# Kernel tuning notes

Measured on AMD Instinct MI355X. Metric: run time of the kernel, lower is better.

## Reference

```python
import jax, jax.numpy as jnp
import numpy as np

B, S, D, H, HID = 8192, 16, 128, 8, 1024
DH = D // H  # 16
GCN, NUMF = 40, 103
EPS = 1e-5

def _make_pe():
    pos = np.arange(S, dtype=np.float64)[:, None]
    i = np.arange(D, dtype=np.float64)[None, :]
    pe = pos / np.power(10000.0, (i // 2 * 2.0) / D)
    pe[:, 0::2] = np.sin(pe[:, 0::2])
    pe[:, 1::2] = np.cos(pe[:, 1::2])
    return jnp.asarray(pe, dtype=jnp.float32)  # [S, D]

PE = _make_pe()

def setup_inputs() -> dict:
    key = jax.random.key(0)
    ks = jax.random.split(key, 16)
    rn = lambda k, shape, s=0.02: (jax.random.normal(k, shape, jnp.float32) * s)
    return {
        "x": jax.random.normal(ks[0], (B, S, D), jnp.float32),
        "gcn_i": jax.random.normal(ks[1], (B, GCN), jnp.float32),
        "num": jax.random.normal(ks[2], (B, NUMF), jnp.float32),
        # two independent encoder layers, params stacked on leading dim
        "Wq": rn(ks[3], (2, D, D)), "bq": jnp.zeros((2, D), jnp.float32),
        "Wk": rn(ks[4], (2, D, D)), "bk": jnp.zeros((2, D), jnp.float32),
        "Wv": rn(ks[5], (2, D, D)), "bv": jnp.zeros((2, D), jnp.float32),
        "Wo": rn(ks[6], (2, D, D)), "bo": jnp.zeros((2, D), jnp.float32),
        "ln1_g": jnp.ones((2, D), jnp.float32), "ln1_b": jnp.zeros((2, D), jnp.float32),
        "W1": rn(ks[7], (2, D, HID)), "b1": jnp.zeros((2, HID), jnp.float32),
        "W2": rn(ks[8], (2, HID, D)), "b2": jnp.zeros((2, D), jnp.float32),
        "ln2_g": jnp.ones((2, D), jnp.float32), "ln2_b": jnp.zeros((2, D), jnp.float32),
        # head
        "Wn": rn(ks[9], (NUMF, D)), "bnum": jnp.zeros((D,), jnp.float32),
        "bn_gamma": jnp.ones((D,), jnp.float32), "bn_beta": jnp.zeros((D,), jnp.float32),
        "Wf": rn(ks[10], (S * D + GCN + D, 1)), "bf": jnp.zeros((1,), jnp.float32),
    }

def _ln(x, g, b):
    m = x.mean(-1, keepdims=True)
    v = ((x - m) ** 2).mean(-1, keepdims=True)
    return (x - m) * jax.lax.rsqrt(v + EPS) * g + b

def reference(x, gcn_i, num, Wq, bq, Wk, bk, Wv, bv, Wo, bo, ln1_g, ln1_b,
              W1, b1, W2, b2, ln2_g, ln2_b, Wn, bnum, bn_gamma, bn_beta, Wf, bf):
    out = x + PE  # positional encoding (dropout = identity in eval)
    scale = DH ** -0.5
    for l in range(2):
        # NOTE: original uses a raw .view(B*H, -1, DH) (no transpose) -- faithful reshape
        q = (out @ Wq[l] + bq[l]).reshape(B * H, S, DH)
        k = (out @ Wk[l] + bk[l]).reshape(B * H, S, DH)
        v = (out @ Wv[l] + bv[l]).reshape(B * H, S, DH)
        attn = jax.nn.softmax(jnp.einsum('nsd,ntd->nst', q, k) * scale, axis=-1)
        ctx = jnp.einsum('nst,ntd->nsd', attn, v).reshape(B, S, D)
        h = _ln(ctx @ Wo[l] + bo[l] + out, ln1_g[l], ln1_b[l])
        ff = jax.nn.relu(h @ W1[l] + b1[l]) @ W2[l] + b2[l]
        out = _ln(ff + h, ln2_g[l], ln2_b[l])
    flat = out.reshape(B, S * D)  # [B, 2048]
    n = num @ Wn + bnum  # [B, 128]
    # BatchNorm1d, training-mode forward (biased batch variance)
    mu = n.mean(0)
    var = ((n - mu) ** 2).mean(0)
    n = (n - mu) * jax.lax.rsqrt(var + EPS) * bn_gamma + bn_beta
    p = jnp.concatenate([flat, gcn_i, n], axis=-1)  # [B, 2216]
    return jax.nn.sigmoid(p @ Wf + bf)
```

## Files before the change

kernel.cpp:

```cpp
#include <hip/hip_runtime.h>
#include <hip/hip_bf16.h>
#include <math.h>

#define B_SZ   8192
#define S_SZ   16
#define D_SZ   128
#define HID_SZ 1024
#define NUMF_SZ 103
#define GCN_SZ 40
#define G_B    4
#define NBLK   (B_SZ / G_B)
#define STRD   136

typedef short bh8 __attribute__((ext_vector_type(8)));
typedef float fx4 __attribute__((ext_vector_type(4)));

__device__ __forceinline__ fx4 mfma16(bh8 a, bh8 b, fx4 c) {
    return __builtin_amdgcn_mfma_f32_16x16x32_bf16(a, b, c, 0, 0, 0);
}

__device__ __forceinline__ unsigned short f2b(float f) {
    unsigned u = __float_as_uint(f);
    return (unsigned short)((u + 0x7fffu + ((u >> 16) & 1u)) >> 16);
}
__device__ __forceinline__ float bu2f(unsigned short u) {
    return __uint_as_float(((unsigned)u) << 16);
}

__global__ __launch_bounds__(256) void prep_weights(
    const float* __restrict__ Wq, const float* __restrict__ Wk,
    const float* __restrict__ Wv, const float* __restrict__ Wo,
    const float* __restrict__ W1, const float* __restrict__ W2,
    unsigned short* __restrict__ WswQ, unsigned short* __restrict__ WswK,
    unsigned short* __restrict__ WswV, unsigned short* __restrict__ WswO,
    unsigned short* __restrict__ Wsw1, unsigned short* __restrict__ Wsw2,
    float* __restrict__ PEt)
{
    int i = blockIdx.x * 256 + threadIdx.x;
    if (i < 2048) {
        int s = i >> 7, c = i & 127;
        float expo = (float)((c >> 1) * 2) * (1.0f / 128.0f);
        float denom = powf(10000.0f, expo);
        float ang = (float)s / denom;
        PEt[i] = (c & 1) ? cosf(ang) : sinf(ang);
    }
    if (i < 2 * 16384) {
        int l = i >> 14, r = i & 16383;
        int nt = r >> 11, ks = (r >> 9) & 3, lane = (r >> 3) & 63, e = r & 7;
        int k = ks * 32 + (lane >> 4) * 8 + e;
        int n = nt * 16 + (lane & 15);
        int s = l * 16384 + k * 128 + n;
        WswQ[i] = f2b(Wq[s]); WswK[i] = f2b(Wk[s]);
        WswV[i] = f2b(Wv[s]); WswO[i] = f2b(Wo[s]);
    }
    {
        int l = i >> 17, r = i & 131071;
        int nt = r >> 11, ks = (r >> 9) & 3, lane = (r >> 3) & 63, e = r & 7;
        int k = ks * 32 + (lane >> 4) * 8 + e;
        int n = nt * 16 + (lane & 15);
        Wsw1[i] = f2b(W1[l * 131072 + k * 1024 + n]);
    }
    {
        int l = i >> 17, r = i & 131071;
        int nt = r >> 14, kt = (r >> 9) & 31, lane = (r >> 3) & 63, e = r & 7;
        int k = kt * 32 + (lane >> 4) * 8 + e;
        int n = nt * 16 + (lane & 15);
        Wsw2[i] = f2b(W2[l * 131072 + k * 128 + n]);
    }
}

__global__ __launch_bounds__(256, 2) void encoder_fused(
    const float* __restrict__ x, const float* __restrict__ gcn,
    const float* __restrict__ bq, const float* __restrict__ bk,
    const float* __restrict__ bv, const float* __restrict__ bo,
    const float* __restrict__ ln1g, const float* __restrict__ ln1b,
    const float* __restrict__ b1, const float* __restrict__ b2p,
    const float* __restrict__ ln2g, const float* __restrict__ ln2b,
    const float* __restrict__ Wf,
    const unsigned short* __restrict__ WswQ, const unsigned short* __restrict__ WswK,
    const unsigned short* __restrict__ WswV, const unsigned short* __restrict__ WswO,
    const unsigned short* __restrict__ Wsw1, const unsigned short* __restrict__ Wsw2,
    const float* __restrict__ PEt,
    float* __restrict__ acc1)
{
    __shared__ unsigned short ACT[64][STRD];
    __shared__ unsigned short Qb[64][STRD];
    __shared__ unsigned short Kb[64][STRD];
    __shared__ unsigned short Vb[64][STRD];
    __shared__ float LNp[64][4][2];
    __shared__ float LNs[64][2];

    const int t = threadIdx.x;
    const int w = t >> 6, lane = t & 63;
    const int q = lane >> 4, ln = lane & 15;
    const int bbase = blockIdx.x * G_B;

    {
        const float4* xb = (const float4*)(x + (size_t)bbase * 2048);
        const float4* pe4 = (const float4*)PEt;
#pragma unroll
        for (int i = 0; i < 8; ++i) {
            int f4 = i * 256 + t;
            float4 xv = xb[f4];
            float4 pv = pe4[f4 & 511];
            int flat = f4 * 4;
            int row = flat >> 7, col = flat & 127;
            ushort4 pk = {f2b(xv.x + pv.x), f2b(xv.y + pv.y),
                          f2b(xv.z + pv.z), f2b(xv.w + pv.w)};
            *(ushort4*)&ACT[row][col] = pk;
        }
    }
    __syncthreads();

    for (int l = 0; l < 2; ++l) {
        {
            bh8 afr[4][4];
#pragma unroll
            for (int mt = 0; mt < 4; ++mt)
#pragma unroll
                for (int ks = 0; ks < 4; ++ks)
                    afr[mt][ks] = *(const bh8*)&ACT[mt * 16 + ln][ks * 32 + q * 8];
            const unsigned short* Wm[3] = {WswQ + l * 16384, WswK + l * 16384, WswV + l * 16384};
            const float* bias3[3] = {bq + l * 128, bk + l * 128, bv + l * 128};
#pragma unroll
            for (int mtx = 0; mtx < 3; ++mtx) {
                unsigned short (*dst)[STRD] = (mtx == 0) ? Qb : (mtx == 1) ? Kb : Vb;
#pragma unroll
                for (int i2 = 0; i2 < 2; ++i2) {
                    int nt = w * 2 + i2;
                    bh8 wfr[4];
#pragma unroll
                    for (int ks = 0; ks < 4; ++ks)
                        wfr[ks] = *(const bh8*)(Wm[mtx] + ((nt * 4 + ks) * 64 + lane) * 8);
                    int n = nt * 16 + ln;
                    float bb = bias3[mtx][n];
#pragma unroll
                    for (int mt = 0; mt < 4; ++mt) {
                        fx4 acc = {0.f, 0.f, 0.f, 0.f};
#pragma unroll
                        for (int ks = 0; ks < 4; ++ks) acc = mfma16(afr[mt][ks], wfr[ks], acc);
#pragma unroll
                        for (int r2 = 0; r2 < 4; ++r2)
                            dst[mt * 16 + q * 4 + r2][n] = f2b(acc[r2] + bb);
                    }
                }
            }
        }
        __syncthreads();

        {
            int base = w * 16;
            int g = lane >> 3, u0 = (lane & 7) * 2;
            float qr[2][16];
#pragma unroll
            for (int h = 0; h < 2; ++h) {
                int u = u0 + h;
                int qsr = base + 2 * g + (u >> 3), qc = (u & 7) * 16;
                bh8 a0 = *(const bh8*)&Qb[qsr][qc];
                bh8 a1 = *(const bh8*)&Qb[qsr][qc + 8];
#pragma unroll
                for (int e = 0; e < 8; ++e) {
                    qr[h][e] = bu2f((unsigned short)a0[e]);
                    qr[h][8 + e] = bu2f((unsigned short)a1[e]);
                }
            }
            float p[2][16];
#pragma unroll
            for (int tp = 0; tp < 16; ++tp) {
                int ksr = base + 2 * g + (tp >> 3), kc = (tp & 7) * 16;
                bh8 k0 = *(const bh8*)&Kb[ksr][kc];
                bh8 k1 = *(const bh8*)&Kb[ksr][kc + 8];
                float d0 = 0.f, d1 = 0.f;
#pragma unroll
                for (int e = 0; e < 8; ++e) {
                    float kv = bu2f((unsigned short)k0[e]);
                    d0 = fmaf(qr[0][e], kv, d0); d1 = fmaf(qr[1][e], kv, d1);
                }
#pragma unroll
                for (int e = 0; e < 8; ++e) {
                    float kv = bu2f((unsigned short)k1[e]);
                    d0 = fmaf(qr[0][8 + e], kv, d0); d1 = fmaf(qr[1][8 + e], kv, d1);
                }
                p[0][tp] = d0 * 0.25f; p[1][tp] = d1 * 0.25f;
            }
#pragma unroll
            for (int h = 0; h < 2; ++h) {
                float mx = -1e30f;
#pragma unroll
                for (int tp = 0; tp < 16; ++tp) mx = fmaxf(mx, p[h][tp]);
                float sum = 0.f;
#pragma unroll
                for (int tp = 0; tp < 16; ++tp) { p[h][tp] = __expf(p[h][tp] - mx); sum += p[h][tp]; }
                float is = 1.0f / sum;
#pragma unroll
                for (int tp = 0; tp < 16; ++tp) p[h][tp] *= is;
            }
            float ctx[2][16];
#pragma unroll
            for (int h = 0; h < 2; ++h)
#pragma unroll
                for (int e = 0; e < 16; ++e) ctx[h][e] = 0.f;
#pragma unroll
            for (int tp = 0; tp < 16; ++tp) {
                int vsr = base + 2 * g + (tp >> 3), vc = (tp & 7) * 16;
                bh8 v0 = *(const bh8*)&Vb[vsr][vc];
                bh8 v1 = *(const bh8*)&Vb[vsr][vc + 8];
#pragma unroll
                for (int e = 0; e < 8; ++e) {
                    float vv = bu2f((unsigned short)v0[e]);
                    ctx[0][e] = fmaf(p[0][tp], vv, ctx[0][e]);
                    ctx[1][e] = fmaf(p[1][tp], vv, ctx[1][e]);
                }
#pragma unroll
                for (int e = 0; e < 8; ++e) {
                    float vv = bu2f((unsigned short)v1[e]);
                    ctx[0][8 + e] = fmaf(p[0][tp], vv, ctx[0][8 + e]);
                    ctx[1][8 + e] = fmaf(p[1][tp], vv, ctx[1][8 + e]);
                }
            }
#pragma unroll
            for (int h = 0; h < 2; ++h) {
                int u = u0 + h;
                int s = base + 2 * g + (u >> 3), dc = (u & 7) * 16;
                bh8 c0, c1;
#pragma unroll
                for (int e = 0; e < 8; ++e) {
                    c0[e] = (short)f2b(ctx[h][e]);
                    c1[e] = (short)f2b(ctx[h][8 + e]);
                }
                *(bh8*)&Qb[s][dc] = c0;
                *(bh8*)&Qb[s][dc + 8] = c1;
            }
        }
        __syncthreads();

        fx4 Cv[2][4];
        {
            bh8 cfr[4][4];
#pragma unroll
            for (int mt = 0; mt < 4; ++mt)
#pragma unroll
                for (int ks = 0; ks < 4; ++ks)
                    cfr[mt][ks] = *(const bh8*)&Qb[mt * 16 + ln][ks * 32 + q * 8];
#pragma unroll
            for (int i2 = 0; i2 < 2; ++i2) {
                int nt = w * 2 + i2, n = nt * 16 + ln;
                bh8 wfr[4];
#pragma unroll
                for (int ks = 0; ks < 4; ++ks)
                    wfr[ks] = *(const bh8*)(WswO + l * 16384 + ((nt * 4 + ks) * 64 + lane) * 8);
                float bb = bo[l * 128 + n];
#pragma unroll
                for (int mt = 0; mt < 4; ++mt) {
                    fx4 acc = {0.f, 0.f, 0.f, 0.f};
#pragma unroll
                    for (int ks = 0; ks < 4; ++ks) acc = mfma16(cfr[mt][ks], wfr[ks], acc);
#pragma unroll
                    for (int r2 = 0; r2 < 4; ++r2)
                        Cv[i2][mt][r2] = acc[r2] + bb +
                            bu2f(ACT[mt * 16 + q * 4 + r2][n]);
                }
            }
        }
#pragma unroll
        for (int mt = 0; mt < 4; ++mt) {
            float s4[4], v4[4];
#pragma unroll
            for (int r2 = 0; r2 < 4; ++r2) {
                float a0 = Cv[0][mt][r2], a1 = Cv[1][mt][r2];
                float s = a0 + a1, v = a0 * a0 + a1 * a1;
#pragma unroll
                for (int m = 1; m < 16; m <<= 1) { s += __shfl_xor(s, m); v += __shfl_xor(v, m); }
                s4[r2] = s; v4[r2] = v;
            }
            if (ln < 8)
                LNp[mt * 16 + q * 4 + (ln >> 1)][w][ln & 1] = (ln & 1) ? v4[ln >> 1] : s4[ln >> 1];
        }
        __syncthreads();
        if (t < 64) {
            float s = LNp[t][0][0] + LNp[t][1][0] + LNp[t][2][0] + LNp[t][3][0];
            float v = LNp[t][0][1] + LNp[t][1][1] + LNp[t][2][1] + LNp[t][3][1];
            float mean = s * (1.0f / 128.0f);
            LNs[t][0] = mean;
            LNs[t][1] = rsqrtf(v * (1.0f / 128.0f) - mean * mean + 1e-5f);
        }
        __syncthreads();
#pragma unroll
        for (int i2 = 0; i2 < 2; ++i2) {
            int n = (w * 2 + i2) * 16 + ln;
            float gg = ln1g[l * 128 + n], be = ln1b[l * 128 + n];
#pragma unroll
            for (int mt = 0; mt < 4; ++mt)
#pragma unroll
                for (int r2 = 0; r2 < 4; ++r2) {
                    int row = mt * 16 + q * 4 + r2;
                    Kb[row][n] = f2b((Cv[i2][mt][r2] - LNs[row][0]) * LNs[row][1] * gg + be);
                }
        }
        __syncthreads();

        bh8 hfr[4][4];
#pragma unroll
        for (int mt = 0; mt < 4; ++mt)
#pragma unroll
            for (int ks = 0; ks < 4; ++ks)
                hfr[mt][ks] = *(const bh8*)&Kb[mt * 16 + ln][ks * 32 + q * 8];
        fx4 f2a[2][4];
#pragma unroll
        for (int i2 = 0; i2 < 2; ++i2)
#pragma unroll
            for (int mt = 0; mt < 4; ++mt) f2a[i2][mt] = fx4{0.f, 0.f, 0.f, 0.f};
        for (int ch = 0; ch < 8; ++ch) {
            bh8 w1fr[2][4];
#pragma unroll
            for (int i2 = 0; i2 < 2; ++i2) {
                int ntg = ch * 8 + w * 2 + i2;
#pragma unroll
                for (int ks = 0; ks < 4; ++ks)
                    w1fr[i2][ks] = *(const bh8*)(Wsw1 + l * 131072 + ((ntg * 4 + ks) * 64 + lane) * 8);
            }
#pragma unroll
            for (int mt = 0; mt < 4; ++mt) {
#pragma unroll
                for (int i2 = 0; i2 < 2; ++i2) {
                    fx4 acc = {0.f, 0.f, 0.f, 0.f};
#pragma unroll
                    for (int ks = 0; ks < 4; ++ks) acc = mfma16(hfr[mt][ks], w1fr[i2][ks], acc);
                    int nl = (w * 2 + i2) * 16 + ln;
                    float bb = b1[l * HID_SZ + ch * 128 + nl];
#pragma unroll
                    for (int r2 = 0; r2 < 4; ++r2) {
                        float vv = acc[r2] + bb;
                        Qb[mt * 16 + q * 4 + r2][nl] = f2b(vv > 0.f ? vv : 0.f);
                    }
                }
            }
            __syncthreads();
            bh8 w2fr[2][4];
#pragma unroll
            for (int i2 = 0; i2 < 2; ++i2)
#pragma unroll
                for (int ks = 0; ks < 4; ++ks)
                    w2fr[i2][ks] = *(const bh8*)(Wsw2 + l * 131072 +
                        (((w * 2 + i2) * 32 + ch * 4 + ks) * 64 + lane) * 8);
#pragma unroll
            for (int mt = 0; mt < 4; ++mt) {
                bh8 ffr[4];
#pragma unroll
                for (int ks = 0; ks < 4; ++ks)
                    ffr[ks] = *(const bh8*)&Qb[mt * 16 + ln][ks * 32 + q * 8];
#pragma unroll
                for (int i2 = 0; i2 < 2; ++i2)
#pragma unroll
                    for (int ks = 0; ks < 4; ++ks)
                        f2a[i2][mt] = mfma16(ffr[ks], w2fr[i2][ks], f2a[i2][mt]);
            }
            __syncthreads();
        }
        fx4 Cv2[2][4];
#pragma unroll
        for (int i2 = 0; i2 < 2; ++i2) {
            int n = (w * 2 + i2) * 16 + ln;
            float bb = b2p[l * 128 + n];
#pragma unroll
            for (int mt = 0; mt < 4; ++mt)
#pragma unroll
                for (int r2 = 0; r2 < 4; ++r2)
                    Cv2[i2][mt][r2] = f2a[i2][mt][r2] + bb +
                        bu2f(Kb[mt * 16 + q * 4 + r2][n]);
        }
#pragma unroll
        for (int mt = 0; mt < 4; ++mt) {
            float s4[4], v4[4];
#pragma unroll
            for (int r2 = 0; r2 < 4; ++r2) {
                float a0 = Cv2[0][mt][r2], a1 = Cv2[1][mt][r2];
                float s = a0 + a1, v = a0 * a0 + a1 * a1;
#pragma unroll
                for (int m = 1; m < 16; m <<= 1) { s += __shfl_xor(s, m); v += __shfl_xor(v, m); }
                s4[r2] = s; v4[r2] = v;
            }
            if (ln < 8)
                LNp[mt * 16 + q * 4 + (ln >> 1)][w][ln & 1] = (ln & 1) ? v4[ln >> 1] : s4[ln >> 1];
        }
        __syncthreads();
        if (t < 64) {
            float s = LNp[t][0][0] + LNp[t][1][0] + LNp[t][2][0] + LNp[t][3][0];
            float v = LNp[t][0][1] + LNp[t][1][1] + LNp[t][2][1] + LNp[t][3][1];
            float mean = s * (1.0f / 128.0f);
            LNs[t][0] = mean;
            LNs[t][1] = rsqrtf(v * (1.0f / 128.0f) - mean * mean + 1e-5f);
        }
        __syncthreads();
#pragma unroll
        for (int i2 = 0; i2 < 2; ++i2) {
            int n = (w * 2 + i2) * 16 + ln;
            float gg = ln2g[l * 128 + n], be = ln2b[l * 128 + n];
#pragma unroll
            for (int mt = 0; mt < 4; ++mt)
#pragma unroll
                for (int r2 = 0; r2 < 4; ++r2) {
                    int row = mt * 16 + q * 4 + r2;
                    ACT[row][n] = f2b((Cv2[i2][mt][r2] - LNs[row][0]) * LNs[row][1] * gg + be);
                }
        }
        __syncthreads();
    }

    {
        int bg = bbase + w;
        float part = 0.f;
        int srow = lane >> 2, c0 = (lane & 3) * 32;
#pragma unroll
        for (int i = 0; i < 4; ++i) {
            bh8 av = *(const bh8*)&ACT[w * 16 + srow][c0 + i * 8];
            int fl = srow * 128 + c0 + i * 8;
#pragma unroll
            for (int e = 0; e < 8; ++e)
                part = fmaf(bu2f((unsigned short)av[e]), Wf[fl + e], part);
        }
        if (lane < GCN_SZ)
            part = fmaf(gcn[(size_t)bg * GCN_SZ + lane], Wf[2048 + lane], part);
#pragma unroll
        for (int off = 32; off; off >>= 1) part += __shfl_xor(part, off);
        if (lane == 0) acc1[bg] = part;
    }
}

__global__ __launch_bounds__(256) void num_stats_kernel(
    const float* __restrict__ num, const float* __restrict__ Wn,
    const float* __restrict__ bnum,
    float* __restrict__ ssum, float* __restrict__ ssq)
{
    __shared__ float NUM[16][NUMF_SZ + 1];
    __shared__ float cred[4][128];
    const int t = threadIdx.x;
    const int b0 = blockIdx.x * 16;
    const int j = t & 127, sg = t >> 7, s0 = sg * 8;

    for (int idx = t; idx < 16 * NUMF_SZ; idx += 256) {
        int r = idx / NUMF_SZ, f = idx - r * NUMF_SZ;
        NUM[r][f] = num[(size_t)(b0 + r) * NUMF_SZ + f];
    }
    __syncthreads();

    float acc[8];
    float bnv = bnum[j];
#pragma unroll
    for (int r = 0; r < 8; ++r) acc[r] = bnv;
    for (int f = 0; f < NUMF_SZ; ++f) {
        float w = Wn[f * 128 + j];
#pragma unroll
        for (int r = 0; r < 8; ++r) acc[r] = fmaf(NUM[s0 + r][f], w, acc[r]);
    }
    float lsum = 0.f, lsq = 0.f;
#pragma unroll
    for (int r = 0; r < 8; ++r) {
        lsum += acc[r];
        lsq = fmaf(acc[r], acc[r], lsq);
    }
    cred[sg][j] = lsum;
    cred[2 + sg][j] = lsq;
    __syncthreads();
    if (sg == 0) atomicAdd(&ssum[j], cred[0][j] + cred[1][j]);
    else         atomicAdd(&ssq[j],  cred[2][j] + cred[3][j]);
}

__global__ __launch_bounds__(128) void final_kernel(
    const float* __restrict__ num, const float* __restrict__ Wn,
    const float* __restrict__ bnum,
    const float* __restrict__ ssum, const float* __restrict__ ssq,
    const float* __restrict__ gamma, const float* __restrict__ beta,
    const float* __restrict__ Wf, const float* __restrict__ bfin,
    const float* __restrict__ acc1, float* __restrict__ out)
{
    const int b = blockIdx.x, jj = threadIdx.x;
    __shared__ float red2[2];
    __shared__ float NUMr[NUMF_SZ];
    if (jj < NUMF_SZ) NUMr[jj] = num[(size_t)b * NUMF_SZ + jj];
    __syncthreads();

    float nv = bnum[jj];
    for (int f = 0; f < NUMF_SZ; ++f)
        nv = fmaf(NUMr[f], Wn[f * 128 + jj], nv);

    float mean = ssum[jj] * (1.0f / (float)B_SZ);
    float var = ssq[jj] * (1.0f / (float)B_SZ) - mean * mean;
    float bnv = (nv - mean) * rsqrtf(var + 1e-5f) * gamma[jj] + beta[jj];
    float v = bnv * Wf[2088 + jj];
#pragma unroll
    for (int o = 32; o; o >>= 1) v += __shfl_down(v, o);
    if ((jj & 63) == 0) red2[jj >> 6] = v;
    __syncthreads();
    if (jj == 0) {
        float z = acc1[b] + red2[0] + red2[1] + bfin[0];
        out[b] = 1.0f / (1.0f + __expf(-z));
    }
}

extern "C" void kernel_launch(void* const* d_in, const int* in_sizes, int n_in,
                              void* d_out, int out_size, void* d_ws, size_t ws_size,
                              hipStream_t stream)
{
    const float* x    = (const float*)d_in[0];
    const float* gcn  = (const float*)d_in[1];
    const float* num  = (const float*)d_in[2];
    const float* Wq   = (const float*)d_in[3];
    const float* bq   = (const float*)d_in[4];
    const float* Wk   = (const float*)d_in[5];
    const float* bk   = (const float*)d_in[6];
    const float* Wv   = (const float*)d_in[7];
    const float* bv   = (const float*)d_in[8];
    const float* Wo   = (const float*)d_in[9];
    const float* bo   = (const float*)d_in[10];
    const float* ln1g = (const float*)d_in[11];
    const float* ln1b = (const float*)d_in[12];
    const float* W1   = (const float*)d_in[13];
    const float* b1   = (const float*)d_in[14];
    const float* W2   = (const float*)d_in[15];
    const float* b2p  = (const float*)d_in[16];
    const float* ln2g = (const float*)d_in[17];
    const float* ln2b = (const float*)d_in[18];
    const float* Wn   = (const float*)d_in[19];
    const float* bnum = (const float*)d_in[20];
    const float* bng  = (const float*)d_in[21];
    const float* bnb  = (const float*)d_in[22];
    const float* Wf   = (const float*)d_in[23];
    const float* bfin = (const float*)d_in[24];

    float* acc1 = (float*)d_ws;
    float* ssum = acc1 + B_SZ;
    float* ssq  = ssum + 128;
    unsigned short* wb = (unsigned short*)((char*)d_ws + 40960);
    unsigned short* WswQ = wb;
    unsigned short* WswK = wb + 32768;
    unsigned short* WswV = wb + 65536;
    unsigned short* WswO = wb + 98304;
    unsigned short* Wsw1 = wb + 131072;
    unsigned short* Wsw2 = wb + 393216;
    float* PEt = (float*)((char*)d_ws + 40960 + 1310720);

    hipMemsetAsync(ssum, 0, 2 * 128 * sizeof(float), stream);
    prep_weights<<<1024, 256, 0, stream>>>(Wq, Wk, Wv, Wo, W1, W2,
        WswQ, WswK, WswV, WswO, Wsw1, Wsw2, PEt);
    encoder_fused<<<NBLK, 256, 0, stream>>>(x, gcn, bq, bk, bv, bo,
        ln1g, ln1b, b1, b2p, ln2g, ln2b, Wf,
        WswQ, WswK, WswV, WswO, Wsw1, Wsw2, PEt, acc1);
    num_stats_kernel<<<B_SZ / 16, 256, 0, stream>>>(num, Wn, bnum, ssum, ssq);
    final_kernel<<<B_SZ, 128, 0, stream>>>(num, Wn, bnum, ssum, ssq, bng, bnb,
        Wf, bfin, acc1, (float*)d_out);
}
```

Before: 491.1 us.

## Drop ACT LDS buffer, keep residual in registers, merge stats into prep

The encoder kernel drops its separate ACT shared buffer and reuses Qb for the activations. The residual is kept in registers (rsd), and the LN statistics reuse LNp, which cuts LDS use enough to raise launch bounds from 2 to 3 blocks per CU. The numeric-feature BatchNorm statistics kernel is folded into the weight-prep launch as extra blocks, and the final kernel now handles 8 rows per block instead of 1. The aim is higher occupancy and fewer, fatter launches, at the risk of register spills under the tighter 3-block bound and an extra sync per layer.

```diff
diff --git a/kernel.cpp b/kernel.cpp
--- a/kernel.cpp
+++ b/kernel.cpp
@@ -27,49 +27,86 @@
     return __uint_as_float(((unsigned)u) << 16);
 }
 
-__global__ __launch_bounds__(256) void prep_weights(
+__global__ __launch_bounds__(256) void prep_and_stats(
     const float* __restrict__ Wq, const float* __restrict__ Wk,
     const float* __restrict__ Wv, const float* __restrict__ Wo,
     const float* __restrict__ W1, const float* __restrict__ W2,
+    const float* __restrict__ num, const float* __restrict__ Wn,
+    const float* __restrict__ bnum,
     unsigned short* __restrict__ WswQ, unsigned short* __restrict__ WswK,
     unsigned short* __restrict__ WswV, unsigned short* __restrict__ WswO,
     unsigned short* __restrict__ Wsw1, unsigned short* __restrict__ Wsw2,
-    float* __restrict__ PEt)
+    float* __restrict__ PEt, float* __restrict__ ssum, float* __restrict__ ssq)
 {
-    int i = blockIdx.x * 256 + threadIdx.x;
-    if (i < 2048) {
-        int s = i >> 7, c = i & 127;
-        float expo = (float)((c >> 1) * 2) * (1.0f / 128.0f);
-        float denom = powf(10000.0f, expo);
-        float ang = (float)s / denom;
-        PEt[i] = (c & 1) ? cosf(ang) : sinf(ang);
-    }
-    if (i < 2 * 16384) {
-        int l = i >> 14, r = i & 16383;
-        int nt = r >> 11, ks = (r >> 9) & 3, lane = (r >> 3) & 63, e = r & 7;
-        int k = ks * 32 + (lane >> 4) * 8 + e;
-        int n = nt * 16 + (lane & 15);
-        int s = l * 16384 + k * 128 + n;
-        WswQ[i] = f2b(Wq[s]); WswK[i] = f2b(Wk[s]);
-        WswV[i] = f2b(Wv[s]); WswO[i] = f2b(Wo[s]);
-    }
-    {
-        int l = i >> 17, r = i & 131071;
-        int nt = r >> 11, ks = (r >> 9) & 3, lane = (r >> 3) & 63, e = r & 7;
-        int k = ks * 32 + (lane >> 4) * 8 + e;
-        int n = nt * 16 + (lane & 15);
-        Wsw1[i] = f2b(W1[l * 131072 + k * 1024 + n]);
-    }
-    {
-        int l = i >> 17, r = i & 131071;
-        int nt = r >> 14, kt = (r >> 9) & 31, lane = (r >> 3) & 63, e = r & 7;
-        int k = kt * 32 + (lane >> 4) * 8 + e;
-        int n = nt * 16 + (lane & 15);
-        Wsw2[i] = f2b(W2[l * 131072 + k * 128 + n]);
-    }
-}
-
-__global__ __launch_bounds__(256, 2) void encoder_fused(
+    if (blockIdx.x < 1024) {
+        int i = blockIdx.x * 256 + threadIdx.x;
+        if (i < 2048) {
+            int s = i >> 7, c = i & 127;
+            float expo = (float)((c >> 1) * 2) * (1.0f / 128.0f);
+            float denom = powf(10000.0f, expo);
+            float ang = (float)s / denom;
+            PEt[i] = (c & 1) ? cosf(ang) : sinf(ang);
+        }
+        if (i < 2 * 16384) {
+            int l = i >> 14, r = i & 16383;
+            int nt = r >> 11, ks = (r >> 9) & 3, lane = (r >> 3) & 63, e = r & 7;
+            int k = ks * 32 + (lane >> 4) * 8 + e;
+            int n = nt * 16 + (lane & 15);
+            int s = l * 16384 + k * 128 + n;
+            WswQ[i] = f2b(Wq[s]); WswK[i] = f2b(Wk[s]);
+            WswV[i] = f2b(Wv[s]); WswO[i] = f2b(Wo[s]);
+        }
+        {
+            int l = i >> 17, r = i & 131071;
+            int nt = r >> 11, ks = (r >> 9) & 3, lane = (r >> 3) & 63, e = r & 7;
+            int k = ks * 32 + (lane >> 4) * 8 + e;
+            int n = nt * 16 + (lane & 15);
+            Wsw1[i] = f2b(W1[l * 131072 + k * 1024 + n]);
+        }
+        {
+            int l = i >> 17, r = i & 131071;
+            int nt = r >> 14, kt = (r >> 9) & 31, lane = (r >> 3) & 63, e = r & 7;
+            int k = kt * 32 + (lane >> 4) * 8 + e;
+            int n = nt * 16 + (lane & 15);
+            Wsw2[i] = f2b(W2[l * 131072 + k * 128 + n]);
+        }
+    } else {
+        __shared__ float NUM[16][NUMF_SZ + 1];
+        __shared__ float cred[4][128];
+        const int t = threadIdx.x;
+        const int b0 = (blockIdx.x - 1024) * 16;
+        const int j = t & 127, sg = t >> 7, s0 = sg * 8;
+
+        for (int idx = t; idx < 16 * NUMF_SZ; idx += 256) {
+            int r = idx / NUMF_SZ, f = idx - r * NUMF_SZ;
+            NUM[r][f] = num[(size_t)(b0 + r) * NUMF_SZ + f];
+        }
+        __syncthreads();
+
+        float acc[8];
+        float bnv = bnum[j];
+#pragma unroll
+        for (int r = 0; r < 8; ++r) acc[r] = bnv;
+        for (int f = 0; f < NUMF_SZ; ++f) {
+            float w = Wn[f * 128 + j];
+#pragma unroll
+            for (int r = 0; r < 8; ++r) acc[r] = fmaf(NUM[s0 + r][f], w, acc[r]);
+        }
+        float lsum = 0.f, lsq = 0.f;
+#pragma unroll
+        for (int r = 0; r < 8; ++r) {
+            lsum += acc[r];
+            lsq = fmaf(acc[r], acc[r], lsq);
+        }
+        cred[sg][j] = lsum;
+        cred[2 + sg][j] = lsq;
+        __syncthreads();
+        if (sg == 0) atomicAdd(&ssum[j], cred[0][j] + cred[1][j]);
+        else         atomicAdd(&ssq[j],  cred[2][j] + cred[3][j]);
+    }
+}
+
+__global__ __launch_bounds__(256, 3) void encoder_fused(
     const float* __restrict__ x, const float* __restrict__ gcn,
     const float* __restrict__ bq, const float* __restrict__ bk,
     const float* __restrict__ bv, const float* __restrict__ bo,
@@ -83,12 +120,10 @@
     const float* __restrict__ PEt,
     float* __restrict__ acc1)
 {
-    __shared__ unsigned short ACT[64][STRD];
     __shared__ unsigned short Qb[64][STRD];
     __shared__ unsigned short Kb[64][STRD];
     __shared__ unsigned short Vb[64][STRD];
     __shared__ float LNp[64][4][2];
-    __shared__ float LNs[64][2];
 
     const int t = threadIdx.x;
     const int w = t >> 6, lane = t & 63;
@@ -107,19 +142,32 @@
             int row = flat >> 7, col = flat & 127;
             ushort4 pk = {f2b(xv.x + pv.x), f2b(xv.y + pv.y),
                           f2b(xv.z + pv.z), f2b(xv.w + pv.w)};
-            *(ushort4*)&ACT[row][col] = pk;
+            *(ushort4*)&Qb[row][col] = pk;
         }
     }
     __syncthreads();
 
+    float rsd[2][4][4];
+#pragma unroll
+    for (int i2 = 0; i2 < 2; ++i2) {
+        int n = (w * 2 + i2) * 16 + ln;
+#pragma unroll
+        for (int mt = 0; mt < 4; ++mt)
+#pragma unroll
+            for (int r2 = 0; r2 < 4; ++r2)
+                rsd[i2][mt][r2] = bu2f(Qb[mt * 16 + q * 4 + r2][n]);
+    }
+
     for (int l = 0; l < 2; ++l) {
+        bh8 afr[4][4];
+#pragma unroll
+        for (int mt = 0; mt < 4; ++mt)
+#pragma unroll
+            for (int ks = 0; ks < 4; ++ks)
+                afr[mt][ks] = *(const bh8*)&Qb[mt * 16 + ln][ks * 32 + q * 8];
+        __syncthreads();
+
         {
-            bh8 afr[4][4];
-#pragma unroll
-            for (int mt = 0; mt < 4; ++mt)
-#pragma unroll
-                for (int ks = 0; ks < 4; ++ks)
-                    afr[mt][ks] = *(const bh8*)&ACT[mt * 16 + ln][ks * 32 + q * 8];
             const unsigned short* Wm[3] = {WswQ + l * 16384, WswK + l * 16384, WswV + l * 16384};
             const float* bias3[3] = {bq + l * 128, bk + l * 128, bv + l * 128};
 #pragma unroll
@@ -257,8 +305,7 @@
                     for (int ks = 0; ks < 4; ++ks) acc = mfma16(cfr[mt][ks], wfr[ks], acc);
 #pragma unroll
                     for (int r2 = 0; r2 < 4; ++r2)
-                        Cv[i2][mt][r2] = acc[r2] + bb +
-                            bu2f(ACT[mt * 16 + q * 4 + r2][n]);
+                        Cv[i2][mt][r2] = acc[r2] + bb + rsd[i2][mt][r2];
                 }
             }
         }
@@ -281,8 +328,9 @@
             float s = LNp[t][0][0] + LNp[t][1][0] + LNp[t][2][0] + LNp[t][3][0];
             float v = LNp[t][0][1] + LNp[t][1][1] + LNp[t][2][1] + LNp[t][3][1];
             float mean = s * (1.0f / 128.0f);
-            LNs[t][0] = mean;
-            LNs[t][1] = rsqrtf(v * (1.0f / 128.0f) - mean * mean + 1e-5f);
+            float inv = rsqrtf(v * (1.0f / 128.0f) - mean * mean + 1e-5f);
+            LNp[t][0][0] = mean;
+            LNp[t][0][1] = inv;
         }
         __syncthreads();
 #pragma unroll
@@ -294,7 +342,7 @@
 #pragma unroll
                 for (int r2 = 0; r2 < 4; ++r2) {
                     int row = mt * 16 + q * 4 + r2;
-                    Kb[row][n] = f2b((Cv[i2][mt][r2] - LNs[row][0]) * LNs[row][1] * gg + be);
+                    Kb[row][n] = f2b((Cv[i2][mt][r2] - LNp[row][0][0]) * LNp[row][0][1] * gg + be);
                 }
         }
         __syncthreads();
@@ -388,8 +436,9 @@
             float s = LNp[t][0][0] + LNp[t][1][0] + LNp[t][2][0] + LNp[t][3][0];
             float v = LNp[t][0][1] + LNp[t][1][1] + LNp[t][2][1] + LNp[t][3][1];
             float mean = s * (1.0f / 128.0f);
-            LNs[t][0] = mean;
-            LNs[t][1] = rsqrtf(v * (1.0f / 128.0f) - mean * mean + 1e-5f);
+            float inv = rsqrtf(v * (1.0f / 128.0f) - mean * mean + 1e-5f);
+            LNp[t][0][0] = mean;
+            LNp[t][0][1] = inv;
         }
         __syncthreads();
 #pragma unroll
@@ -401,7 +450,10 @@
 #pragma unroll
                 for (int r2 = 0; r2 < 4; ++r2) {
                     int row = mt * 16 + q * 4 + r2;
-                    ACT[row][n] = f2b((Cv2[i2][mt][r2] - LNs[row][0]) * LNs[row][1] * gg + be);
+                    unsigned short us =
+                        f2b((Cv2[i2][mt][r2] - LNp[row][0][0]) * LNp[row][0][1] * gg + be);
+                    Qb[row][n] = us;
+                    rsd[i2][mt][r2] = bu2f(us);
                 }
         }
         __syncthreads();
@@ -413,7 +465,7 @@
         int srow = lane >> 2, c0 = (lane & 3) * 32;
 #pragma unroll
         for (int i = 0; i < 4; ++i) {
-            bh8 av = *(const bh8*)&ACT[w * 16 + srow][c0 + i * 8];
+            bh8 av = *(const bh8*)&Qb[w * 16 + srow][c0 + i * 8];
             int fl = srow * 128 + c0 + i * 8;
 #pragma unroll
             for (int e = 0; e < 8; ++e)
@@ -425,45 +477,6 @@
         for (int off = 32; off; off >>= 1) part += __shfl_xor(part, off);
         if (lane == 0) acc1[bg] = part;
     }
-}
-
-__global__ __launch_bounds__(256) void num_stats_kernel(
-    const float* __restrict__ num, const float* __restrict__ Wn,
-    const float* __restrict__ bnum,
-    float* __restrict__ ssum, float* __restrict__ ssq)
-{
-    __shared__ float NUM[16][NUMF_SZ + 1];
-    __shared__ float cred[4][128];
-    const int t = threadIdx.x;
-    const int b0 = blockIdx.x * 16;
-    const int j = t & 127, sg = t >> 7, s0 = sg * 8;
-
-    for (int idx = t; idx < 16 * NUMF_SZ; idx += 256) {
-        int r = idx / NUMF_SZ, f = idx - r * NUMF_SZ;
-        NUM[r][f] = num[(size_t)(b0 + r) * NUMF_SZ + f];
-    }
-    __syncthreads();
-
-    float acc[8];
-    float bnv = bnum[j];
-#pragma unroll
-    for (int r = 0; r < 8; ++r) acc[r] = bnv;
-    for (int f = 0; f < NUMF_SZ; ++f) {
-        float w = Wn[f * 128 + j];
-#pragma unroll
-        for (int r = 0; r < 8; ++r) acc[r] = fmaf(NUM[s0 + r][f], w, acc[r]);
-    }
-    float lsum = 0.f, lsq = 0.f;
-#pragma unroll
-    for (int r = 0; r < 8; ++r) {
-        lsum += acc[r];
-        lsq = fmaf(acc[r], acc[r], lsq);
-    }
-    cred[sg][j] = lsum;
-    cred[2 + sg][j] = lsq;
-    __syncthreads();
-    if (sg == 0) atomicAdd(&ssum[j], cred[0][j] + cred[1][j]);
-    else         atomicAdd(&ssq[j],  cred[2][j] + cred[3][j]);
 }
 
 __global__ __launch_bounds__(128) void final_kernel(
@@ -474,27 +487,43 @@
     const float* __restrict__ Wf, const float* __restrict__ bfin,
     const float* __restrict__ acc1, float* __restrict__ out)
 {
-    const int b = blockIdx.x, jj = threadIdx.x;
-    __shared__ float red2[2];
-    __shared__ float NUMr[NUMF_SZ];
-    if (jj < NUMF_SZ) NUMr[jj] = num[(size_t)b * NUMF_SZ + jj];
+    const int b0 = blockIdx.x * 8, jj = threadIdx.x;
+    __shared__ float NUMr[8][NUMF_SZ];
+    __shared__ float redF[2][8];
+    for (int idx = jj; idx < 8 * NUMF_SZ; idx += 128) {
+        int r = idx / NUMF_SZ, f = idx - r * NUMF_SZ;
+        NUMr[r][f] = num[(size_t)(b0 + r) * NUMF_SZ + f];
+    }
     __syncthreads();
 
-    float nv = bnum[jj];
-    for (int f = 0; f < NUMF_SZ; ++f)
-        nv = fmaf(NUMr[f], Wn[f * 128 + jj], nv);
-
+    float nv[8];
+    float bn = bnum[jj];
+#pragma unroll
+    for (int r = 0; r < 8; ++r) nv[r] = bn;
+    for (int f = 0; f < NUMF_SZ; ++f) {
+        float wv = Wn[f * 128 + jj];
+#pragma unroll
+        for (int r = 0; r < 8; ++r) nv[r] = fmaf(NUMr[r][f], wv, nv[r]);
+    }
     float mean = ssum[jj] * (1.0f / (float)B_SZ);
     float var = ssq[jj] * (1.0f / (float)B_SZ) - mean * mean;
-    float bnv = (nv - mean) * rsqrtf(var + 1e-5f) * gamma[jj] + beta[jj];
-    float v = bnv * Wf[2088 + jj];
-#pragma unroll
-    for (int o = 32; o; o >>= 1) v += __shfl_down(v, o);
-    if ((jj & 63) == 0) red2[jj >> 6] = v;
+    float scale = rsqrtf(var + 1e-5f) * gamma[jj];
+    float bet = beta[jj];
+    float wf = Wf[2088 + jj];
+    float v[8];
+#pragma unroll
+    for (int r = 0; r < 8; ++r) v[r] = ((nv[r] - mean) * scale + bet) * wf;
+#pragma unroll
+    for (int off = 32; off; off >>= 1)
+#pragma unroll
+        for (int r = 0; r < 8; ++r) v[r] += __shfl_xor(v[r], off);
+    if ((jj & 63) == 0)
+#pragma unroll
+        for (int r = 0; r < 8; ++r) redF[jj >> 6][r] = v[r];
     __syncthreads();
-    if (jj == 0) {
-        float z = acc1[b] + red2[0] + red2[1] + bfin[0];
-        out[b] = 1.0f / (1.0f + __expf(-z));
+    if (jj < 8) {
+        float z = acc1[b0 + jj] + redF[0][jj] + redF[1][jj] + bfin[0];
+        out[b0 + jj] = 1.0f / (1.0f + __expf(-z));
     }
 }
 
@@ -541,12 +570,12 @@
     float* PEt = (float*)((char*)d_ws + 40960 + 1310720);
 
     hipMemsetAsync(ssum, 0, 2 * 128 * sizeof(float), stream);
-    prep_weights<<<1024, 256, 0, stream>>>(Wq, Wk, Wv, Wo, W1, W2,
-        WswQ, WswK, WswV, WswO, Wsw1, Wsw2, PEt);
+    prep_and_stats<<<1536, 256, 0, stream>>>(Wq, Wk, Wv, Wo, W1, W2,
+        num, Wn, bnum,
+        WswQ, WswK, WswV, WswO, Wsw1, Wsw2, PEt, ssum, ssq);
     encoder_fused<<<NBLK, 256, 0, stream>>>(x, gcn, bq, bk, bv, bo,
         ln1g, ln1b, b1, b2p, ln2g, ln2b, Wf,
         WswQ, WswK, WswV, WswO, Wsw1, Wsw2, PEt, acc1);
-    num_stats_kernel<<<B_SZ / 16, 256, 0, stream>>>(num, Wn, bnum, ssum, ssq);
-    final_kernel<<<B_SZ, 128, 0, stream>>>(num, Wn, bnum, ssum, ssq, bng, bnb,
+    final_kernel<<<B_SZ / 8, 128, 0, stream>>>(num, Wn, bnum, ssum, ssq, bng, bnb,
         Wf, bfin, acc1, (float*)d_out);
 }
```

Measured after the change: 615.5 us. 1.25x slower.
